# Optimization experiments

Measured on AMD Instinct MI355X. Metric: run time of the kernel, lower is better.

The kernel has to match this reference:

```python
import jax, jax.numpy as jnp
import numpy as np

N_SENSORY = 784   # MNIST sensory nodes (init_modes prints 784)
LR_X = 0.5        # lr_x
T = 10            # T_test fixed-point iterations


def setup_inputs() -> dict:
    key = jax.random.key(0)
    k1, k2, k3, k4 = jax.random.split(key, 4)
    B, N, E = 128, 2000, 131072
    x = jax.random.normal(k1, (B, N), dtype=jnp.float32)
    src = jax.random.randint(k2, (E,), 0, N)
    tgt = jax.random.randint(k3, (E,), 0, N)
    edge_index = jnp.stack([src, tgt]).astype(jnp.int32)  # [2, E], shared across batch
    # w init: fill 0.001 + 1e-4 noise (see _reset_params), gathered per-edge
    w_edges = (0.001 + 0.0001 * jax.random.normal(k4, (E,), dtype=jnp.float32))
    # test mode: update internal + supervised nodes (>= 784); sensory errors zeroed
    # because use_input_error=False -> same mask used for errors.
    update_mask = (jnp.arange(N) >= N_SENSORY).astype(jnp.float32)
    return {"x": x, "edge_index": edge_index, "w_edges": w_edges,
            "update_mask": update_mask}


def reference(x, edge_index, w_edges, update_mask):
    # x: [B, N] node values; edge_index: [2, E] (row 0 = source, row 1 = target)
    src, tgt = edge_index[0], edge_index[1]
    N = x.shape[1]

    seg = lambda vals, idx: jax.ops.segment_sum(vals, idx, num_segments=N)
    dfdx = lambda v: 1.0 - jnp.tanh(v) ** 2  # tanh_derivative

    def step(xc, _):
        fx = jnp.tanh(xc)
        # PredictionMessagePassing (flow=target_to_source, aggr=add):
        #   mu[src] += f(x[tgt]) * w_edge
        mu = jax.vmap(lambda fb: seg(fb[tgt] * w_edges, src))(fx)       # [B, N]
        # use_input_error=False: sensory errors zeroed
        err = (xc - mu) * update_mask                                    # [B, N]
        # GradientMessagePassing (flow=source_to_target, aggr=add):
        #   aggr[tgt] += dfdx(x[tgt]) * err[src] * w_edge ; dx = err - aggr
        agg = jax.vmap(lambda eb: seg(eb[src] * w_edges, tgt))(err)      # [B, N]
        dx = err - dfdx(xc) * agg
        # gradient step on unclamped (internal + label) nodes only
        xc = xc - LR_X * dx * update_mask
        return xc, None

    x_final, _ = jax.lax.scan(step, x, None, length=T)
    return x_final
```

## Files before the change

kernel.cpp:

```cpp
#include <hip/hip_runtime.h>

#define NITER 10
#define NBLK 250
#define CAP_H 96


__device__ __forceinline__ uint32_t aload(const uint32_t* p) {
  return __hip_atomic_load(p, __ATOMIC_RELAXED, __HIP_MEMORY_SCOPE_AGENT);
}
__device__ __forceinline__ void astore(uint32_t* p, uint32_t v) {
  __hip_atomic_store(p, v, __ATOMIC_RELAXED, __HIP_MEMORY_SCOPE_AGENT);
}
__device__ __forceinline__ float bf2f_lo(uint32_t v) { return __uint_as_float(v << 16); }
__device__ __forceinline__ float bf2f_hi(uint32_t v) { return __uint_as_float(v & 0xFFFF0000u); }
__device__ __forceinline__ uint32_t f2bf_bits(float f) {
  uint32_t b = __float_as_uint(f);
  b += 0x7FFFu + ((b >> 16) & 1u);
  return b >> 16;
}
__device__ __forceinline__ uint32_t pack_bf16x2(float lo, float hi) {
  return f2bf_bits(lo) | (f2bf_bits(hi) << 16);
}

__device__ __forceinline__ void mbar(uint32_t* ms, uint32_t target) {
  asm volatile("s_waitcnt vmcnt(0)" ::: "memory");
  __syncthreads();
  if (threadIdx.x < 64) {
    if (threadIdx.x == 0) astore(&ms[blockIdx.x], target);
    for (;;) {
      bool ok = true;
      if (threadIdx.x < 8) ok = (aload(&ms[threadIdx.x]) >= target);
      if (__all(ok)) break;
      __builtin_amdgcn_s_sleep(2);
    }
  }
  __syncthreads();
  asm volatile("" ::: "memory");
}


__global__ __launch_bounds__(1024) void hist_scan_kernel(
    const int* __restrict__ src, const int* __restrict__ tgt, const float* __restrict__ mask,
    int* __restrict__ partS, int* __restrict__ partT,
    int* __restrict__ offS, int* __restrict__ offT,
    int* __restrict__ curS, int* __restrict__ curT,
    int* __restrict__ actv, int* __restrict__ nactg,
    uint32_t* __restrict__ ms, int E, int N) {
  __shared__ int h[4096];
  const int bid = blockIdx.x, tid = threadIdx.x;

  for (int i = tid; i < 2 * N; i += 1024) h[i] = 0;
  __syncthreads();
  const int chunk = E / 8;
  const int base = bid * chunk;
  const int cnt = (bid == 7) ? (E - 7 * chunk) : chunk;
  for (int k = tid; k < cnt; k += 1024) {
    int e = base + k;
    int s = src[e], t = tgt[e];
    if (mask[s] != 0.f) {
      atomicAdd(&h[s], 1);
      if (mask[t] != 0.f) atomicAdd(&h[N + t], 1);
    }
  }
  __syncthreads();
  for (int i = tid; i < N; i += 1024) {
    astore((uint32_t*)&partS[bid * 2048 + i], (uint32_t)h[i]);
    astore((uint32_t*)&partT[bid * 2048 + i], (uint32_t)h[N + i]);
  }
  mbar(ms, 1);

  if (bid < 3) {
    int* tsum = h;
    int v2[2];
    int s = 0;
#pragma unroll
    for (int i2 = 0; i2 < 2; ++i2) {
      int idx = tid * 2 + i2;
      int c = 0;
      if (idx < N) {
        if (bid == 2) {
          c = (mask[idx] != 0.f) ? 1 : 0;
        } else {
          const int* part = bid ? partT : partS;
#pragma unroll
          for (int k = 0; k < 8; ++k) c += (int)aload((const uint32_t*)&part[k * 2048 + idx]);
        }
      }
      v2[i2] = s;
      s += c;
    }
    __syncthreads();
    tsum[tid] = s;
    __syncthreads();
    for (int d = 1; d < 1024; d <<= 1) {
      int t = (tid >= d) ? tsum[tid - d] : 0;
      __syncthreads();
      tsum[tid] += t;
      __syncthreads();
    }
    int tbase = tsum[tid] - s;
    if (bid == 2) {
#pragma unroll
      for (int i2 = 0; i2 < 2; ++i2) {
        int idx = tid * 2 + i2;
        if (idx < N && mask[idx] != 0.f) actv[tbase + v2[i2]] = idx;
      }
      if (tid == 1023) *nactg = tsum[1023];
    } else {
      int* off = bid ? offT : offS;
      int* cur = bid ? curT : curS;
#pragma unroll
      for (int i2 = 0; i2 < 2; ++i2) {
        int idx = tid * 2 + i2;
        if (idx < N) {
          int o = tbase + v2[i2];
          off[idx] = o;
          cur[idx] = o;
        } else if (idx == N) {
          off[idx] = tbase + v2[i2];
        }
      }
    }
  }
}


__global__ void scatter_kernel(const float* __restrict__ x,
                               const int* __restrict__ src, const int* __restrict__ tgt,
                               const float* __restrict__ w, const float* __restrict__ mask,
                               int* __restrict__ curS, int* __restrict__ curT,
                               uint32_t* __restrict__ edgeS, uint32_t* __restrict__ edgeT,
                               uint32_t* __restrict__ fx32, float* __restrict__ out,
                               int E, int N) {
  const int e = blockIdx.x * 256 + threadIdx.x;
  if (e < E) {
    int s = src[e], t = tgt[e];
    if (mask[s] != 0.f) {
      uint32_t wb = __float_as_uint(w[e]);
      wb = (wb + 0x7FFFu + ((wb >> 16) & 1u)) & 0xFFFF0000u;
      int p = atomicAdd(&curS[s], 1);
      edgeS[p] = (uint32_t)t | wb;
      if (mask[t] != 0.f) {
        int q = atomicAdd(&curT[t], 1);
        edgeT[q] = (uint32_t)s | wb;
      }
    }
  }
  const int gs = (int)gridDim.x * 256;
  for (int g = e; g < N * 64; g += gs) {
    int n = g >> 6;
    if (mask[n] == 0.f) {
      int l = g & 63;
      fx32[g] = pack_bf16x2(tanhf(x[(2 * l) * N + n]), tanhf(x[(2 * l + 1) * N + n]));
    }
  }
  for (int g = e; g < N * 128; g += gs) {
    int b = g / N, n = g - b * N;
    if (mask[n] == 0.f) out[g] = x[g];
  }
}


__device__ __forceinline__ void gbar(uint32_t* bar, uint32_t target) {
  asm volatile("s_waitcnt vmcnt(0)" ::: "memory");
  __syncthreads();
  if (threadIdx.x == 0) {
    const int nb = (int)gridDim.x;
    const int li = blockIdx.x & 15;
    uint32_t* leaf = bar + li * 16;
    uint32_t* root = bar + 256;
    uint32_t* gen = bar + 272;
    const int q = nb >> 4, r = nb & 15;
    const uint32_t leafsz = (uint32_t)(li < r ? q + 1 : q);
    uint32_t lo = __hip_atomic_fetch_add(leaf, 1u, __ATOMIC_RELAXED, __HIP_MEMORY_SCOPE_AGENT);
    if (lo == leafsz - 1) {
      astore(leaf, 0u);
      asm volatile("s_waitcnt vmcnt(0)" ::: "memory");
      uint32_t ro = __hip_atomic_fetch_add(root, 1u, __ATOMIC_RELAXED, __HIP_MEMORY_SCOPE_AGENT);
      if (ro == 15u) {
        astore(root, 0u);
        asm volatile("s_waitcnt vmcnt(0)" ::: "memory");
        astore(gen, target);
      }
    }
    while (aload(gen) < target) __builtin_amdgcn_s_sleep(2);
  }
  __syncthreads();
  asm volatile("" ::: "memory");
}

__device__ __forceinline__ void gq_lds(const uint32_t* __restrict__ se, int len,
                                       const uint32_t* buf, int lane, float& o0, float& o1) {
  float a0[8], a1[8];
#pragma unroll
  for (int j = 0; j < 8; ++j) { a0[j] = 0.f; a1[j] = 0.f; }
#pragma unroll 2
  for (int p = 0; p < len; p += 8) {
    uint32_t e[8];
#pragma unroll
    for (int j = 0; j < 8; ++j) e[j] = se[p + j];
    uint32_t v[8];
#pragma unroll
    for (int j = 0; j < 8; ++j) v[j] = aload(&buf[((e[j] & 0xFFFFu) << 6) + lane]);
#pragma unroll
    for (int j = 0; j < 8; ++j) {
      float wj = __uint_as_float(e[j] & 0xFFFF0000u);
      a0[j] = fmaf(wj, bf2f_lo(v[j]), a0[j]);
      a1[j] = fmaf(wj, bf2f_hi(v[j]), a1[j]);
    }
  }
  o0 = ((a0[0] + a0[1]) + (a0[2] + a0[3])) + ((a0[4] + a0[5]) + (a0[6] + a0[7]));
  o1 = ((a1[0] + a1[1]) + (a1[2] + a1[3])) + ((a1[4] + a1[5]) + (a1[6] + a1[7]));
}

__device__ __forceinline__ void gq_glb(const uint32_t* __restrict__ ed, int len,
                                       const uint32_t* buf, int lane, float& o0, float& o1) {
  float a0[8], a1[8];
#pragma unroll
  for (int j = 0; j < 8; ++j) { a0[j] = 0.f; a1[j] = 0.f; }
#pragma unroll 2
  for (int p = 0; p < len; p += 8) {
    uint32_t e[8], v[8];
#pragma unroll
    for (int j = 0; j < 8; ++j) {
      bool ok = (p + j) < len;
      e[j] = ok ? ed[p + j] : 0u;
      v[j] = ok ? aload(&buf[((e[j] & 0xFFFFu) << 6) + lane]) : 0u;
    }
#pragma unroll
    for (int j = 0; j < 8; ++j) {
      float wj = __uint_as_float(e[j] & 0xFFFF0000u);
      a0[j] = fmaf(wj, bf2f_lo(v[j]), a0[j]);
      a1[j] = fmaf(wj, bf2f_hi(v[j]), a1[j]);
    }
  }
  o0 = ((a0[0] + a0[1]) + (a0[2] + a0[3])) + ((a0[4] + a0[5]) + (a0[6] + a0[7]));
  o1 = ((a1[0] + a1[1]) + (a1[2] + a1[3])) + ((a1[4] + a1[5]) + (a1[6] + a1[7]));
}

__global__ __launch_bounds__(1024, 4) void pc_main(
    const float* __restrict__ x, float* __restrict__ out,
    const int* __restrict__ offS, const uint32_t* __restrict__ edS,
    const int* __restrict__ offT, const uint32_t* __restrict__ edT,
    const int* __restrict__ actv, const int* __restrict__ nactg,
    uint32_t* fx32, uint32_t* err32, const float* __restrict__ mask,
    uint32_t* bar, int N) {
  __shared__ uint32_t sE[2][16][CAP_H];
  __shared__ float2 psum[8][64];
  const int tid = threadIdx.x, wid = tid >> 6, lane = tid & 63;
  const int ps = wid >> 1, sub = wid & 1;
  const int nact = *nactg;
  const int p = ps * (int)gridDim.x + (int)blockIdx.x;
  const bool act = (p < nact);

  int n = 0, i = 0, aS = 0, qlS = 0, qpS = 0, aT = 0, qlT = 0, qpT = 0;
  bool fS = true, fT = true;
  float m = 0.f, x0 = 0.f, x1 = 0.f, fx0 = 0.f, fx1 = 0.f, e0 = 0.f, e1 = 0.f;

  if (act) {
    n = actv[p];
    i = (n << 6) + lane;
    const int s0 = offS[n], degS = offS[n + 1] - s0;
    const int t0 = offT[n], degT = offT[n + 1] - t0;
    aS = s0 + ((degS * sub) >> 1); qlS = (s0 + ((degS * (sub + 1)) >> 1)) - aS;
    aT = t0 + ((degT * sub) >> 1); qlT = (t0 + ((degT * (sub + 1)) >> 1)) - aT;
    qpS = (qlS + 7) & ~7; qpT = (qlT + 7) & ~7;
    fS = (qpS <= CAP_H); fT = (qpT <= CAP_H);
    if (fS)
      for (int k = lane; k < qpS; k += 64) sE[0][wid][k] = (k < qlS) ? edS[aS + k] : 0u;
    if (fT)
      for (int k = lane; k < qpT; k += 64) sE[1][wid][k] = (k < qlT) ? edT[aT + k] : 0u;
    if (sub == 0) {
      m = mask[n];
      x0 = x[(2 * lane) * N + n];
      x1 = x[(2 * lane + 1) * N + n];
      fx0 = tanhf(x0);
      fx1 = tanhf(x1);
      astore(&fx32[i], pack_bf16x2(fx0, fx1));
    }
  }
  uint32_t gen = 0;
  gbar(bar, ++gen);

  for (int it = 0; it < NITER; ++it) {
    float p0 = 0.f, p1 = 0.f;
    if (act) {
      if (fS) gq_lds(&sE[0][wid][0], qpS, fx32, lane, p0, p1);
      else    gq_glb(edS + aS, qlS, fx32, lane, p0, p1);
      if (sub) psum[ps][lane] = make_float2(p0, p1);
    }
    __syncthreads();
    if (act && sub == 0) {
      float2 q = psum[ps][lane];
      e0 = (x0 - (p0 + q.x)) * m;
      e1 = (x1 - (p1 + q.y)) * m;
      astore(&err32[i], pack_bf16x2(e0, e1));
    }
    gbar(bar, ++gen);

    if (act) {
      if (fT) gq_lds(&sE[1][wid][0], qpT, err32, lane, p0, p1);
      else    gq_glb(edT + aT, qlT, err32, lane, p0, p1);
      if (sub) psum[ps][lane] = make_float2(p0, p1);
    }
    __syncthreads();
    if (act && sub == 0) {
      float2 q = psum[ps][lane];
      const float ag0 = p0 + q.x, ag1 = p1 + q.y;
      const float dx0 = e0 - (1.f - fx0 * fx0) * ag0;
      const float dx1 = e1 - (1.f - fx1 * fx1) * ag1;
      x0 -= 0.5f * dx0 * m;
      x1 -= 0.5f * dx1 * m;
      fx0 = tanhf(x0);
      fx1 = tanhf(x1);
      if (it < NITER - 1) astore(&fx32[i], pack_bf16x2(fx0, fx1));
    }
    if (it < NITER - 1) gbar(bar, ++gen);
  }

  if (act && sub == 0) {
    out[(2 * lane) * N + n] = x0;
    out[(2 * lane + 1) * N + n] = x1;
  }
}


extern "C" void kernel_launch(void* const* d_in, const int* in_sizes, int n_in,
                              void* d_out, int out_size, void* d_ws, size_t ws_size,
                              hipStream_t stream) {
  const float* x = (const float*)d_in[0];
  const int* ei = (const int*)d_in[1];
  const float* w = (const float*)d_in[2];
  const float* mask = (const float*)d_in[3];
  int E = in_sizes[2];
  int N = in_sizes[3];
  const int* src = ei;
  const int* tgt = ei + E;
  float* out = (float*)d_out;

  size_t off = 0;
  auto alloc = [&](size_t bytes) -> void* {
    off = (off + 255) & ~(size_t)255;
    void* p = (char*)d_ws + off;
    off += bytes;
    return p;
  };
  uint32_t* edgeS = (uint32_t*)alloc((size_t)E * 4);
  uint32_t* edgeT = (uint32_t*)alloc((size_t)E * 4);
  int* partS = (int*)alloc(8 * 2048 * 4);
  int* partT = (int*)alloc(8 * 2048 * 4);
  int* offS = (int*)alloc(2048 * 4);
  int* offT = (int*)alloc(2048 * 4);
  int* curS = (int*)alloc(2048 * 4);
  int* curT = (int*)alloc(2048 * 4);
  int* actv = (int*)alloc(2048 * 4);
  int* nactg = (int*)alloc(64 * 4);
  uint32_t* fx32 = (uint32_t*)alloc((size_t)N * 64 * 4);
  uint32_t* err32 = (uint32_t*)alloc((size_t)N * 64 * 4);
  uint32_t* bar = (uint32_t*)alloc(512 * 4);
  uint32_t* ms = (uint32_t*)alloc(64 * 4);

  hipMemsetAsync(bar, 0, (512 + 64) * 4, stream);

  hist_scan_kernel<<<8, 1024, 0, stream>>>(src, tgt, mask, partS, partT, offS, offT, curS, curT,
                                           actv, nactg, ms, E, N);
  scatter_kernel<<<(E + 255) / 256, 256, 0, stream>>>(x, src, tgt, w, mask, curS, curT, edgeS,
                                                      edgeT, fx32, out, E, N);
  pc_main<<<NBLK, 1024, 0, stream>>>(x, out, offS, edgeS, offT, edgeT, actv, nactg, fx32, err32,
                                     mask, bar, N);
}
```

Measured before the change: 187.0 us.

## Fuse histogram, scatter and solver into one persistent kernel with centralized barrier

Merges the histogram/scan kernel, the edge scatter kernel and the main iteration kernel into a single persistent 250-block launch. Grid-wide barriers separate the phases. The histogram is spread over 32 blocks instead of 8. The tree barrier is replaced by a centralized one where block 0 polls all slots and publishes a generation word. This removes two kernel launches and their gaps. In exchange, the edge scatter now runs on only 250 blocks, and a single master block polling 250 slots may add latency at every one of the ~20 barriers.

```diff
diff --git a/kernel.cpp b/kernel.cpp
--- a/kernel.cpp
+++ b/kernel.cpp
@@ -2,6 +2,7 @@
 
 #define NITER 10
 #define NBLK 250
+#define HB 32
 #define CAP_H 96
 
 
@@ -22,52 +23,119 @@
   return f2bf_bits(lo) | (f2bf_bits(hi) << 16);
 }
 
-__device__ __forceinline__ void mbar(uint32_t* ms, uint32_t target) {
+__device__ __forceinline__ void gbar(uint32_t* slots, uint32_t* gen, uint32_t target) {
   asm volatile("s_waitcnt vmcnt(0)" ::: "memory");
   __syncthreads();
-  if (threadIdx.x < 64) {
-    if (threadIdx.x == 0) astore(&ms[blockIdx.x], target);
-    for (;;) {
-      bool ok = true;
-      if (threadIdx.x < 8) ok = (aload(&ms[threadIdx.x]) >= target);
-      if (__all(ok)) break;
-      __builtin_amdgcn_s_sleep(2);
+  if (blockIdx.x == 0) {
+    if (threadIdx.x < 64) {
+      for (;;) {
+        bool ok = true;
+        for (int i = threadIdx.x; i < NBLK; i += 64)
+          ok &= (i == 0) || (aload(&slots[i]) >= target);
+        if (__all(ok)) break;
+        __builtin_amdgcn_s_sleep(1);
+      }
+      if (threadIdx.x == 0) astore(gen, target);
+    }
+  } else {
+    if (threadIdx.x == 0) {
+      astore(&slots[blockIdx.x], target);
+      while (aload(gen) < target) __builtin_amdgcn_s_sleep(2);
     }
   }
   __syncthreads();
   asm volatile("" ::: "memory");
 }
 
-
-__global__ __launch_bounds__(1024) void hist_scan_kernel(
-    const int* __restrict__ src, const int* __restrict__ tgt, const float* __restrict__ mask,
+__device__ __forceinline__ void gq_lds(const uint32_t* __restrict__ se, int len,
+                                       const uint32_t* buf, int lane, float& o0, float& o1) {
+  float a0[8], a1[8];
+#pragma unroll
+  for (int j = 0; j < 8; ++j) { a0[j] = 0.f; a1[j] = 0.f; }
+#pragma unroll 2
+  for (int p = 0; p < len; p += 8) {
+    uint32_t e[8];
+#pragma unroll
+    for (int j = 0; j < 8; ++j) e[j] = se[p + j];
+    uint32_t v[8];
+#pragma unroll
+    for (int j = 0; j < 8; ++j) v[j] = aload(&buf[((e[j] & 0xFFFFu) << 6) + lane]);
+#pragma unroll
+    for (int j = 0; j < 8; ++j) {
+      float wj = __uint_as_float(e[j] & 0xFFFF0000u);
+      a0[j] = fmaf(wj, bf2f_lo(v[j]), a0[j]);
+      a1[j] = fmaf(wj, bf2f_hi(v[j]), a1[j]);
+    }
+  }
+  o0 = ((a0[0] + a0[1]) + (a0[2] + a0[3])) + ((a0[4] + a0[5]) + (a0[6] + a0[7]));
+  o1 = ((a1[0] + a1[1]) + (a1[2] + a1[3])) + ((a1[4] + a1[5]) + (a1[6] + a1[7]));
+}
+
+__device__ __forceinline__ void gq_glb(const uint32_t* __restrict__ ed, int len,
+                                       const uint32_t* buf, int lane, float& o0, float& o1) {
+  float a0[8], a1[8];
+#pragma unroll
+  for (int j = 0; j < 8; ++j) { a0[j] = 0.f; a1[j] = 0.f; }
+#pragma unroll 2
+  for (int p = 0; p < len; p += 8) {
+    uint32_t e[8], v[8];
+#pragma unroll
+    for (int j = 0; j < 8; ++j) {
+      bool ok = (p + j) < len;
+      e[j] = ok ? aload(&ed[p + j]) : 0u;
+      v[j] = ok ? aload(&buf[((e[j] & 0xFFFFu) << 6) + lane]) : 0u;
+    }
+#pragma unroll
+    for (int j = 0; j < 8; ++j) {
+      float wj = __uint_as_float(e[j] & 0xFFFF0000u);
+      a0[j] = fmaf(wj, bf2f_lo(v[j]), a0[j]);
+      a1[j] = fmaf(wj, bf2f_hi(v[j]), a1[j]);
+    }
+  }
+  o0 = ((a0[0] + a0[1]) + (a0[2] + a0[3])) + ((a0[4] + a0[5]) + (a0[6] + a0[7]));
+  o1 = ((a1[0] + a1[1]) + (a1[2] + a1[3])) + ((a1[4] + a1[5]) + (a1[6] + a1[7]));
+}
+
+
+__global__ __launch_bounds__(1024, 4) void pc_all(
+    const float* __restrict__ x, float* __restrict__ out,
+    const int* __restrict__ src, const int* __restrict__ tgt,
+    const float* __restrict__ w, const float* __restrict__ mask,
     int* __restrict__ partS, int* __restrict__ partT,
     int* __restrict__ offS, int* __restrict__ offT,
     int* __restrict__ curS, int* __restrict__ curT,
     int* __restrict__ actv, int* __restrict__ nactg,
-    uint32_t* __restrict__ ms, int E, int N) {
+    uint32_t* __restrict__ edgeS, uint32_t* __restrict__ edgeT,
+    uint32_t* fx32, uint32_t* err32, uint32_t* barbuf, int E, int N) {
   __shared__ int h[4096];
+  __shared__ uint32_t sE[2][16][CAP_H];
+  __shared__ float2 psum[8][64];
+  uint32_t* slots = barbuf;
+  uint32_t* gen = barbuf + 288;
+
   const int bid = blockIdx.x, tid = threadIdx.x;
-
-  for (int i = tid; i < 2 * N; i += 1024) h[i] = 0;
-  __syncthreads();
-  const int chunk = E / 8;
-  const int base = bid * chunk;
-  const int cnt = (bid == 7) ? (E - 7 * chunk) : chunk;
-  for (int k = tid; k < cnt; k += 1024) {
-    int e = base + k;
-    int s = src[e], t = tgt[e];
-    if (mask[s] != 0.f) {
-      atomicAdd(&h[s], 1);
-      if (mask[t] != 0.f) atomicAdd(&h[N + t], 1);
-    }
-  }
-  __syncthreads();
-  for (int i = tid; i < N; i += 1024) {
-    astore((uint32_t*)&partS[bid * 2048 + i], (uint32_t)h[i]);
-    astore((uint32_t*)&partT[bid * 2048 + i], (uint32_t)h[N + i]);
-  }
-  mbar(ms, 1);
+  const int wid = tid >> 6, lane = tid & 63;
+
+  if (bid < HB) {
+    for (int i = tid; i < 2 * N; i += 1024) h[i] = 0;
+    __syncthreads();
+    const int chunk = (E + HB - 1) / HB;
+    const int base = bid * chunk;
+    const int end = min(base + chunk, E);
+    for (int e = base + tid; e < end; e += 1024) {
+      int s = src[e], t = tgt[e];
+      if (mask[s] != 0.f) {
+        atomicAdd(&h[s], 1);
+        if (mask[t] != 0.f) atomicAdd(&h[N + t], 1);
+      }
+    }
+    __syncthreads();
+    for (int i = tid; i < N; i += 1024) {
+      astore((uint32_t*)&partS[bid * 2048 + i], (uint32_t)h[i]);
+      astore((uint32_t*)&partT[bid * 2048 + i], (uint32_t)h[N + i]);
+    }
+  }
+  gbar(slots, gen, 1);
 
   if (bid < 3) {
     int* tsum = h;
@@ -81,9 +149,8 @@
         if (bid == 2) {
           c = (mask[idx] != 0.f) ? 1 : 0;
         } else {
-          const int* part = bid ? partT : partS;
-#pragma unroll
-          for (int k = 0; k < 8; ++k) c += (int)aload((const uint32_t*)&part[k * 2048 + idx]);
+          const uint32_t* part = (const uint32_t*)(bid ? partT : partS);
+          for (int k = 0; k < HB; ++k) c += (int)aload(&part[k * 2048 + idx]);
         }
       }
       v2[i2] = s;
@@ -103,9 +170,10 @@
 #pragma unroll
       for (int i2 = 0; i2 < 2; ++i2) {
         int idx = tid * 2 + i2;
-        if (idx < N && mask[idx] != 0.f) actv[tbase + v2[i2]] = idx;
-      }
-      if (tid == 1023) *nactg = tsum[1023];
+        if (idx < N && mask[idx] != 0.f)
+          astore((uint32_t*)&actv[tbase + v2[i2]], (uint32_t)idx);
+      }
+      if (tid == 1023) astore((uint32_t*)nactg, (uint32_t)tsum[1023]);
     } else {
       int* off = bid ? offT : offS;
       int* cur = bid ? curT : curS;
@@ -114,162 +182,54 @@
         int idx = tid * 2 + i2;
         if (idx < N) {
           int o = tbase + v2[i2];
-          off[idx] = o;
-          cur[idx] = o;
+          astore((uint32_t*)&off[idx], (uint32_t)o);
+          astore((uint32_t*)&cur[idx], (uint32_t)o);
         } else if (idx == N) {
-          off[idx] = tbase + v2[i2];
+          astore((uint32_t*)&off[idx], (uint32_t)(tbase + v2[i2]));
         }
       }
     }
   }
-}
-
-
-__global__ void scatter_kernel(const float* __restrict__ x,
-                               const int* __restrict__ src, const int* __restrict__ tgt,
-                               const float* __restrict__ w, const float* __restrict__ mask,
-                               int* __restrict__ curS, int* __restrict__ curT,
-                               uint32_t* __restrict__ edgeS, uint32_t* __restrict__ edgeT,
-                               uint32_t* __restrict__ fx32, float* __restrict__ out,
-                               int E, int N) {
-  const int e = blockIdx.x * 256 + threadIdx.x;
-  if (e < E) {
-    int s = src[e], t = tgt[e];
-    if (mask[s] != 0.f) {
-      uint32_t wb = __float_as_uint(w[e]);
-      wb = (wb + 0x7FFFu + ((wb >> 16) & 1u)) & 0xFFFF0000u;
-      int p = atomicAdd(&curS[s], 1);
-      edgeS[p] = (uint32_t)t | wb;
-      if (mask[t] != 0.f) {
-        int q = atomicAdd(&curT[t], 1);
-        edgeT[q] = (uint32_t)s | wb;
-      }
-    }
-  }
-  const int gs = (int)gridDim.x * 256;
-  for (int g = e; g < N * 64; g += gs) {
-    int n = g >> 6;
-    if (mask[n] == 0.f) {
-      int l = g & 63;
-      fx32[g] = pack_bf16x2(tanhf(x[(2 * l) * N + n]), tanhf(x[(2 * l + 1) * N + n]));
-    }
-  }
-  for (int g = e; g < N * 128; g += gs) {
-    int b = g / N, n = g - b * N;
-    if (mask[n] == 0.f) out[g] = x[g];
-  }
-}
-
-
-__device__ __forceinline__ void gbar(uint32_t* bar, uint32_t target) {
-  asm volatile("s_waitcnt vmcnt(0)" ::: "memory");
-  __syncthreads();
-  if (threadIdx.x == 0) {
-    const int nb = (int)gridDim.x;
-    const int li = blockIdx.x & 15;
-    uint32_t* leaf = bar + li * 16;
-    uint32_t* root = bar + 256;
-    uint32_t* gen = bar + 272;
-    const int q = nb >> 4, r = nb & 15;
-    const uint32_t leafsz = (uint32_t)(li < r ? q + 1 : q);
-    uint32_t lo = __hip_atomic_fetch_add(leaf, 1u, __ATOMIC_RELAXED, __HIP_MEMORY_SCOPE_AGENT);
-    if (lo == leafsz - 1) {
-      astore(leaf, 0u);
-      asm volatile("s_waitcnt vmcnt(0)" ::: "memory");
-      uint32_t ro = __hip_atomic_fetch_add(root, 1u, __ATOMIC_RELAXED, __HIP_MEMORY_SCOPE_AGENT);
-      if (ro == 15u) {
-        astore(root, 0u);
-        asm volatile("s_waitcnt vmcnt(0)" ::: "memory");
-        astore(gen, target);
-      }
-    }
-    while (aload(gen) < target) __builtin_amdgcn_s_sleep(2);
-  }
-  __syncthreads();
-  asm volatile("" ::: "memory");
-}
-
-__device__ __forceinline__ void gq_lds(const uint32_t* __restrict__ se, int len,
-                                       const uint32_t* buf, int lane, float& o0, float& o1) {
-  float a0[8], a1[8];
-#pragma unroll
-  for (int j = 0; j < 8; ++j) { a0[j] = 0.f; a1[j] = 0.f; }
-#pragma unroll 2
-  for (int p = 0; p < len; p += 8) {
-    uint32_t e[8];
-#pragma unroll
-    for (int j = 0; j < 8; ++j) e[j] = se[p + j];
-    uint32_t v[8];
-#pragma unroll
-    for (int j = 0; j < 8; ++j) v[j] = aload(&buf[((e[j] & 0xFFFFu) << 6) + lane]);
-#pragma unroll
-    for (int j = 0; j < 8; ++j) {
-      float wj = __uint_as_float(e[j] & 0xFFFF0000u);
-      a0[j] = fmaf(wj, bf2f_lo(v[j]), a0[j]);
-      a1[j] = fmaf(wj, bf2f_hi(v[j]), a1[j]);
-    }
-  }
-  o0 = ((a0[0] + a0[1]) + (a0[2] + a0[3])) + ((a0[4] + a0[5]) + (a0[6] + a0[7]));
-  o1 = ((a1[0] + a1[1]) + (a1[2] + a1[3])) + ((a1[4] + a1[5]) + (a1[6] + a1[7]));
-}
-
-__device__ __forceinline__ void gq_glb(const uint32_t* __restrict__ ed, int len,
-                                       const uint32_t* buf, int lane, float& o0, float& o1) {
-  float a0[8], a1[8];
-#pragma unroll
-  for (int j = 0; j < 8; ++j) { a0[j] = 0.f; a1[j] = 0.f; }
-#pragma unroll 2
-  for (int p = 0; p < len; p += 8) {
-    uint32_t e[8], v[8];
-#pragma unroll
-    for (int j = 0; j < 8; ++j) {
-      bool ok = (p + j) < len;
-      e[j] = ok ? ed[p + j] : 0u;
-      v[j] = ok ? aload(&buf[((e[j] & 0xFFFFu) << 6) + lane]) : 0u;
-    }
-#pragma unroll
-    for (int j = 0; j < 8; ++j) {
-      float wj = __uint_as_float(e[j] & 0xFFFF0000u);
-      a0[j] = fmaf(wj, bf2f_lo(v[j]), a0[j]);
-      a1[j] = fmaf(wj, bf2f_hi(v[j]), a1[j]);
-    }
-  }
-  o0 = ((a0[0] + a0[1]) + (a0[2] + a0[3])) + ((a0[4] + a0[5]) + (a0[6] + a0[7]));
-  o1 = ((a1[0] + a1[1]) + (a1[2] + a1[3])) + ((a1[4] + a1[5]) + (a1[6] + a1[7]));
-}
-
-__global__ __launch_bounds__(1024, 4) void pc_main(
-    const float* __restrict__ x, float* __restrict__ out,
-    const int* __restrict__ offS, const uint32_t* __restrict__ edS,
-    const int* __restrict__ offT, const uint32_t* __restrict__ edT,
-    const int* __restrict__ actv, const int* __restrict__ nactg,
-    uint32_t* fx32, uint32_t* err32, const float* __restrict__ mask,
-    uint32_t* bar, int N) {
-  __shared__ uint32_t sE[2][16][CAP_H];
-  __shared__ float2 psum[8][64];
-  const int tid = threadIdx.x, wid = tid >> 6, lane = tid & 63;
+  gbar(slots, gen, 2);
+
+  {
+    const int chunk = (E + NBLK - 1) / NBLK;
+    const int base = bid * chunk;
+    const int end = min(base + chunk, E);
+    for (int e = base + tid; e < end; e += 1024) {
+      int s = src[e], t = tgt[e];
+      if (mask[s] != 0.f) {
+        uint32_t wb = __float_as_uint(w[e]);
+        wb = (wb + 0x7FFFu + ((wb >> 16) & 1u)) & 0xFFFF0000u;
+        int p = atomicAdd(&curS[s], 1);
+        astore(&edgeS[p], (uint32_t)t | wb);
+        if (mask[t] != 0.f) {
+          int q = atomicAdd(&curT[t], 1);
+          astore(&edgeT[q], (uint32_t)s | wb);
+        }
+      }
+    }
+  }
+
   const int ps = wid >> 1, sub = wid & 1;
-  const int nact = *nactg;
-  const int p = ps * (int)gridDim.x + (int)blockIdx.x;
+  const int nact = (int)aload((const uint32_t*)nactg);
+  const int p = ps * NBLK + bid;
   const bool act = (p < nact);
-
   int n = 0, i = 0, aS = 0, qlS = 0, qpS = 0, aT = 0, qlT = 0, qpT = 0;
   bool fS = true, fT = true;
   float m = 0.f, x0 = 0.f, x1 = 0.f, fx0 = 0.f, fx1 = 0.f, e0 = 0.f, e1 = 0.f;
 
   if (act) {
-    n = actv[p];
+    n = (int)aload((const uint32_t*)&actv[p]);
     i = (n << 6) + lane;
-    const int s0 = offS[n], degS = offS[n + 1] - s0;
-    const int t0 = offT[n], degT = offT[n + 1] - t0;
+    const uint32_t* offSu = (const uint32_t*)offS;
+    const uint32_t* offTu = (const uint32_t*)offT;
+    const int s0 = (int)aload(&offSu[n]), degS = (int)aload(&offSu[n + 1]) - s0;
+    const int t0 = (int)aload(&offTu[n]), degT = (int)aload(&offTu[n + 1]) - t0;
     aS = s0 + ((degS * sub) >> 1); qlS = (s0 + ((degS * (sub + 1)) >> 1)) - aS;
     aT = t0 + ((degT * sub) >> 1); qlT = (t0 + ((degT * (sub + 1)) >> 1)) - aT;
     qpS = (qlS + 7) & ~7; qpT = (qlT + 7) & ~7;
     fS = (qpS <= CAP_H); fT = (qpT <= CAP_H);
-    if (fS)
-      for (int k = lane; k < qpS; k += 64) sE[0][wid][k] = (k < qlS) ? edS[aS + k] : 0u;
-    if (fT)
-      for (int k = lane; k < qpT; k += 64) sE[1][wid][k] = (k < qlT) ? edT[aT + k] : 0u;
     if (sub == 0) {
       m = mask[n];
       x0 = x[(2 * lane) * N + n];
@@ -279,14 +239,32 @@
       astore(&fx32[i], pack_bf16x2(fx0, fx1));
     }
   }
-  uint32_t gen = 0;
-  gbar(bar, ++gen);
-
+  for (int g = bid * 1024 + tid; g < N * 64; g += NBLK * 1024) {
+    int nn = g >> 6;
+    if (mask[nn] == 0.f) {
+      int l = g & 63;
+      astore(&fx32[g], pack_bf16x2(tanhf(x[(2 * l) * N + nn]), tanhf(x[(2 * l + 1) * N + nn])));
+    }
+  }
+  for (int g = bid * 1024 + tid; g < N * 128; g += NBLK * 1024) {
+    int b = g / N, nn = g - b * N;
+    if (mask[nn] == 0.f) out[g] = x[g];
+  }
+  gbar(slots, gen, 3);
+
+  if (act) {
+    if (fS)
+      for (int k = lane; k < qpS; k += 64) sE[0][wid][k] = (k < qlS) ? aload(&edgeS[aS + k]) : 0u;
+    if (fT)
+      for (int k = lane; k < qpT; k += 64) sE[1][wid][k] = (k < qlT) ? aload(&edgeT[aT + k]) : 0u;
+  }
+
+  uint32_t g = 3;
   for (int it = 0; it < NITER; ++it) {
     float p0 = 0.f, p1 = 0.f;
     if (act) {
       if (fS) gq_lds(&sE[0][wid][0], qpS, fx32, lane, p0, p1);
-      else    gq_glb(edS + aS, qlS, fx32, lane, p0, p1);
+      else    gq_glb(edgeS + aS, qlS, fx32, lane, p0, p1);
       if (sub) psum[ps][lane] = make_float2(p0, p1);
     }
     __syncthreads();
@@ -296,11 +274,11 @@
       e1 = (x1 - (p1 + q.y)) * m;
       astore(&err32[i], pack_bf16x2(e0, e1));
     }
-    gbar(bar, ++gen);
+    gbar(slots, gen, ++g);
 
     if (act) {
       if (fT) gq_lds(&sE[1][wid][0], qpT, err32, lane, p0, p1);
-      else    gq_glb(edT + aT, qlT, err32, lane, p0, p1);
+      else    gq_glb(edgeT + aT, qlT, err32, lane, p0, p1);
       if (sub) psum[ps][lane] = make_float2(p0, p1);
     }
     __syncthreads();
@@ -315,7 +293,7 @@
       fx1 = tanhf(x1);
       if (it < NITER - 1) astore(&fx32[i], pack_bf16x2(fx0, fx1));
     }
-    if (it < NITER - 1) gbar(bar, ++gen);
+    if (it < NITER - 1) gbar(slots, gen, ++g);
   }
 
   if (act && sub == 0) {
@@ -347,8 +325,8 @@
   };
   uint32_t* edgeS = (uint32_t*)alloc((size_t)E * 4);
   uint32_t* edgeT = (uint32_t*)alloc((size_t)E * 4);
-  int* partS = (int*)alloc(8 * 2048 * 4);
-  int* partT = (int*)alloc(8 * 2048 * 4);
+  int* partS = (int*)alloc((size_t)HB * 2048 * 4);
+  int* partT = (int*)alloc((size_t)HB * 2048 * 4);
   int* offS = (int*)alloc(2048 * 4);
   int* offT = (int*)alloc(2048 * 4);
   int* curS = (int*)alloc(2048 * 4);
@@ -357,15 +335,11 @@
   int* nactg = (int*)alloc(64 * 4);
   uint32_t* fx32 = (uint32_t*)alloc((size_t)N * 64 * 4);
   uint32_t* err32 = (uint32_t*)alloc((size_t)N * 64 * 4);
-  uint32_t* bar = (uint32_t*)alloc(512 * 4);
-  uint32_t* ms = (uint32_t*)alloc(64 * 4);
-
-  hipMemsetAsync(bar, 0, (512 + 64) * 4, stream);
-
-  hist_scan_kernel<<<8, 1024, 0, stream>>>(src, tgt, mask, partS, partT, offS, offT, curS, curT,
-                                           actv, nactg, ms, E, N);
-  scatter_kernel<<<(E + 255) / 256, 256, 0, stream>>>(x, src, tgt, w, mask, curS, curT, edgeS,
-                                                      edgeT, fx32, out, E, N);
-  pc_main<<<NBLK, 1024, 0, stream>>>(x, out, offS, edgeS, offT, edgeT, actv, nactg, fx32, err32,
-                                     mask, bar, N);
-}
+  uint32_t* barbuf = (uint32_t*)alloc(512 * 4);
+
+  hipMemsetAsync(barbuf, 0, 512 * 4, stream);
+
+  pc_all<<<NBLK, 1024, 0, stream>>>(x, out, src, tgt, w, mask, partS, partT, offS, offT,
+                                    curS, curT, actv, nactg, edgeS, edgeT, fx32, err32,
+                                    barbuf, E, N);
+}
```

Measured after the change: 163.5 us. -12.6%, faster.
